# Performance work log

Measured on AMD Instinct MI355X. Metric: run time of the kernel, lower is better.

## Reference

```python
import jax, jax.numpy as jnp
import numpy as np

# Power-of-two, per-tensor, signed fake quantization (brevitas CustomQuant):
# scale = 2^ceil(log2(max|x| / int_max)), restrict POWER_OF_TWO, stats MAX,
# signed, narrow_range=False -> int range [-2^(b-1), 2^(b-1)-1].
# Weights use ROUND, activations use FLOOR (CustomSignedActQuant).

def _fake_quant(x, bits, rnd_fn):
    int_max = 2.0 ** (bits - 1) - 1.0   # 127 for 8-bit
    int_min = -(2.0 ** (bits - 1))      # -128
    max_abs = jnp.max(jnp.abs(x))
    scale = 2.0 ** jnp.ceil(jnp.log2(jnp.maximum(max_abs, 1e-10) / int_max))
    q = jnp.clip(rnd_fn(x / scale), int_min, int_max) * scale
    # straight-through estimator (quant-dequant forward, identity backward)
    return x + jax.lax.stop_gradient(q - x)


def setup_inputs() -> dict:
    key = jax.random.key(0)
    ks = jax.random.split(key, 7)
    B, C, H, W, P = 16, 728, 64, 64, 728
    x = jax.random.normal(ks[0], (B, C, H, W), jnp.float32)
    w_dw = jax.random.normal(ks[1], (C, 1, 3, 3), jnp.float32) * 0.1   # depthwise, groups=C
    w_pw = jax.random.normal(ks[2], (P, C, 1, 1), jnp.float32) * 0.05  # pointwise 1x1
    gamma = 1.0 + 0.1 * jax.random.normal(ks[3], (C,), jnp.float32)
    beta = 0.1 * jax.random.normal(ks[4], (C,), jnp.float32)
    run_mean = 0.1 * jax.random.normal(ks[5], (C,), jnp.float32)
    run_var = 0.5 + jax.random.uniform(ks[6], (C,), jnp.float32)
    return {"x": x, "w_dw": w_dw, "w_pw": w_pw, "gamma": gamma,
            "beta": beta, "run_mean": run_mean, "run_var": run_var}


def reference(x, w_dw, w_pw, gamma, beta, run_mean, run_var):
    C = x.shape[1]
    eps = 1e-5
    # fixed_padding: kernel=3, dilation=1 -> pad_total=2 -> (1,1) each side
    xp = jnp.pad(x, ((0, 0), (0, 0), (1, 1), (1, 1)))
    # quantized depthwise conv (groups = inplanes)
    wq = _fake_quant(w_dw, 8, jnp.round)
    y = jax.lax.conv_general_dilated(
        xp, wq, window_strides=(1, 1), padding='VALID',
        dimension_numbers=('NCHW', 'OIHW', 'NCHW'),
        feature_group_count=C)
    # BatchNorm2d (eval mode, running stats)
    inv = gamma / jnp.sqrt(run_var + eps)                # [C]
    y = y * inv[:, None, None] + (beta - run_mean * inv)[:, None, None]
    # quantized identity on activations (FLOOR)
    y = _fake_quant(y, 8, jnp.floor)
    # quantized pointwise 1x1 conv
    wpq = _fake_quant(w_pw, 8, jnp.round)
    out = jnp.einsum('bchw,oc->bohw', y, wpq[:, :, 0, 0])
    return out
```

## Files before the change

kernel.cpp:

```cpp
#include <hip/hip_runtime.h>

#define C_IN 728
#define NB   16
#define HH   64
#define WW   64
#define HW   4096
#define KPAD 736
#define MPAD 768

typedef __bf16 bf16x8 __attribute__((ext_vector_type(8)));
typedef float  f32x4  __attribute__((ext_vector_type(4)));

__device__ __forceinline__ float p2scale(unsigned bits, float int_max) {
    float ma = __uint_as_float(bits);
    float v = fmaxf(ma, 1e-10f) / int_max;
    int e; float m = frexpf(v, &e);
    if (m == 0.5f) e -= 1;
    return ldexpf(1.0f, e);
}

__global__ void init_slots(unsigned* slots) {
    if (threadIdx.x < 3) slots[threadIdx.x] = 0u;
}

__device__ __forceinline__ float block_max(float v) {
    #pragma unroll
    for (int off = 32; off; off >>= 1) v = fmaxf(v, __shfl_down(v, off));
    __shared__ float red[4];
    int lane = threadIdx.x & 63, wv = threadIdx.x >> 6;
    if (lane == 0) red[wv] = v;
    __syncthreads();
    return fmaxf(fmaxf(red[0], red[1]), fmaxf(red[2], red[3]));
}

__global__ __launch_bounds__(256) void maxabs_kernel(const float* __restrict__ p, int n,
                                                     unsigned* slot) {
    float v = 0.f;
    for (int i = blockIdx.x * 256 + threadIdx.x; i < n; i += gridDim.x * 256)
        v = fmaxf(v, fabsf(p[i]));
    float m = block_max(v);
    if (threadIdx.x == 0)
        atomicMax(slot, __float_as_uint(m));
}

__global__ __launch_bounds__(256) void quant_dw(const float* __restrict__ w,
                                                float* __restrict__ wq,
                                                const unsigned* __restrict__ slots) {
    int i = blockIdx.x * 256 + threadIdx.x;
    if (i >= C_IN * 9) return;
    float s = p2scale(slots[0], 127.f);
    float k = fminf(fmaxf(rintf(w[i] / s), -128.f), 127.f);
    wq[i] = k * s;
}

__global__ __launch_bounds__(256) void dwconv_bn(const float* __restrict__ x,
                                                 const float* __restrict__ wq,
                                                 const float* __restrict__ gamma,
                                                 const float* __restrict__ beta,
                                                 const float* __restrict__ rmean,
                                                 const float* __restrict__ rvar,
                                                 float* __restrict__ y,
                                                 float* __restrict__ partial) {
    __shared__ __align__(16) float tile[HW];
    const int c = blockIdx.x, b = blockIdx.y, t = threadIdx.x;
    const float* xp = x + ((size_t)b * C_IN + c) * HW;

    const float4* xv = (const float4*)xp;
    float4* tv = (float4*)tile;
    #pragma unroll
    for (int i = 0; i < 4; ++i) tv[t + i * 256] = xv[t + i * 256];

    float wk[9];
    #pragma unroll
    for (int j = 0; j < 9; ++j) wk[j] = wq[c * 9 + j];
    const float inv  = gamma[c] / sqrtf(rvar[c] + 1e-5f);
    const float bias = beta[c] - rmean[c] * inv;
    __syncthreads();

    float* yp = y + ((size_t)b * C_IN + c) * HW;
    float vmax = 0.f;
    #pragma unroll
    for (int i = 0; i < 16; ++i) {
        const int p = t + i * 256;
        const int h = p >> 6, wc = p & 63;
        float acc = 0.f;
        #pragma unroll
        for (int dh = -1; dh <= 1; ++dh) {
            const int hh = h + dh;
            if ((unsigned)hh < (unsigned)HH) {
                const int base = hh << 6;
                if (wc > 0)  acc += tile[base + wc - 1] * wk[(dh + 1) * 3 + 0];
                acc += tile[base + wc] * wk[(dh + 1) * 3 + 1];
                if (wc < 63) acc += tile[base + wc + 1] * wk[(dh + 1) * 3 + 2];
            }
        }
        const float val = acc * inv + bias;
        yp[p] = val;
        vmax = fmaxf(vmax, fabsf(val));
    }
    const float m = block_max(vmax);
    if (t == 0) partial[b * C_IN + c] = m;
}

__global__ __launch_bounds__(256) void reduce_partial(const float* __restrict__ p, int n,
                                                      unsigned* __restrict__ slot) {
    float v = 0.f;
    for (int i = threadIdx.x; i < n; i += 256) v = fmaxf(v, p[i]);
    float m = block_max(v);
    if (threadIdx.x == 0) *slot = __float_as_uint(m);
}

__global__ __launch_bounds__(256) void quant_wpw(const float* __restrict__ w,
                                                 unsigned short* __restrict__ wq,
                                                 const unsigned* __restrict__ slots) {
    int i = blockIdx.x * 256 + threadIdx.x;
    if (i >= MPAD * KPAD) return;
    int o = i / KPAD, c = i % KPAD;
    float k = 0.f;
    if (o < C_IN && c < C_IN) {
        float s = p2scale(slots[1], 127.f);
        k = fminf(fmaxf(rintf(w[o * C_IN + c] / s), -128.f), 127.f);
    }
    wq[i] = (unsigned short)(__float_as_uint(k) >> 16);
}

__global__ __launch_bounds__(256) void transpose_quant_y(const float* __restrict__ y,
                                                         unsigned short* __restrict__ yq,
                                                         const unsigned* __restrict__ slots) {
    __shared__ float tile[32][33];
    int tx = threadIdx.x & 31, ty = threadIdx.x >> 5;
    int hw0 = blockIdx.x * 32, c0 = blockIdx.y * 32, b = blockIdx.z;
    float inv_s = 1.0f / p2scale(slots[2], 127.f);

    #pragma unroll
    for (int i = 0; i < 32; i += 8) {
        int c = c0 + ty + i;
        float v = (c < C_IN) ? y[((size_t)(b * C_IN + c)) * HW + hw0 + tx] : 0.f;
        tile[ty + i][tx] = v;
    }
    __syncthreads();
    #pragma unroll
    for (int i = 0; i < 32; i += 8) {
        int hw = hw0 + ty + i;
        int c  = c0 + tx;
        float k = 0.f;
        if (c < C_IN)
            k = fminf(fmaxf(floorf(tile[tx][ty + i] * inv_s), -128.f), 127.f);
        yq[((size_t)b * HW + hw) * KPAD + c] = (unsigned short)(__float_as_uint(k) >> 16);
    }
}

__global__ __launch_bounds__(256) void gemm_kernel(const unsigned short* __restrict__ Wq,
                                                   const unsigned short* __restrict__ Yq,
                                                   float* __restrict__ out,
                                                   const unsigned* __restrict__ slots) {
    __shared__ __align__(16) unsigned short As[128 * 32];
    __shared__ __align__(16) unsigned short Bs[128 * 32];
    const int t = threadIdx.x;
    const int w = t >> 6, l = t & 63;
    const int r = l & 15, q = l >> 4;
    const int wr = w >> 1, wc = w & 1;
    const int m0 = blockIdx.y * 128;
    const int n0 = blockIdx.x * 128;
    const int b  = blockIdx.z;

    const unsigned short* Ag = Wq + (size_t)m0 * KPAD;
    const unsigned short* Bg = Yq + ((size_t)b * HW + n0) * KPAD;

    const int sm0 = t >> 2;
    const int sm1 = 64 + sm0;
    const int sko = (t & 3) * 8;

    f32x4 acc[4][4];
    #pragma unroll
    for (int i = 0; i < 4; ++i)
        #pragma unroll
        for (int j = 0; j < 4; ++j) acc[i][j] = (f32x4){0.f, 0.f, 0.f, 0.f};

    for (int k0 = 0; k0 < KPAD; k0 += 32) {
        __builtin_amdgcn_global_load_lds(
            (const __attribute__((address_space(1))) void*)(Ag + (size_t)sm0 * KPAD + k0 + sko),
            (__attribute__((address_space(3))) void*)(As + w * 512), 16, 0, 0);
        __builtin_amdgcn_global_load_lds(
            (const __attribute__((address_space(1))) void*)(Ag + (size_t)sm1 * KPAD + k0 + sko),
            (__attribute__((address_space(3))) void*)(As + 2048 + w * 512), 16, 0, 0);
        __builtin_amdgcn_global_load_lds(
            (const __attribute__((address_space(1))) void*)(Bg + (size_t)sm0 * KPAD + k0 + sko),
            (__attribute__((address_space(3))) void*)(Bs + w * 512), 16, 0, 0);
        __builtin_amdgcn_global_load_lds(
            (const __attribute__((address_space(1))) void*)(Bg + (size_t)sm1 * KPAD + k0 + sko),
            (__attribute__((address_space(3))) void*)(Bs + 2048 + w * 512), 16, 0, 0);
        __syncthreads();

        bf16x8 af[4], bfr[4];
        #pragma unroll
        for (int fm = 0; fm < 4; ++fm)
            af[fm] = *(const bf16x8*)(As + (wr * 64 + fm * 16 + r) * 32 + q * 8);
        #pragma unroll
        for (int fn = 0; fn < 4; ++fn)
            bfr[fn] = *(const bf16x8*)(Bs + (wc * 64 + fn * 16 + r) * 32 + q * 8);
        #pragma unroll
        for (int fm = 0; fm < 4; ++fm)
            #pragma unroll
            for (int fn = 0; fn < 4; ++fn)
                acc[fm][fn] = __builtin_amdgcn_mfma_f32_16x16x32_bf16(
                    af[fm], bfr[fn], acc[fm][fn], 0, 0, 0);
        __syncthreads();
    }

    const float stot = p2scale(slots[1], 127.f) * p2scale(slots[2], 127.f);
    #pragma unroll
    for (int fm = 0; fm < 4; ++fm) {
        int o = m0 + wr * 64 + fm * 16 + q * 4;
        #pragma unroll
        for (int fn = 0; fn < 4; ++fn) {
            int hw = n0 + wc * 64 + fn * 16 + r;
            float* op = out + ((size_t)b * C_IN + o) * HW + hw;
            #pragma unroll
            for (int reg = 0; reg < 4; ++reg) {
                if (o + reg < C_IN) op[(size_t)reg * HW] = acc[fm][fn][reg] * stot;
            }
        }
    }
}

extern "C" void kernel_launch(void* const* d_in, const int* in_sizes, int n_in,
                              void* d_out, int out_size, void* d_ws, size_t ws_size,
                              hipStream_t stream) {
    const float* x     = (const float*)d_in[0];
    const float* w_dw  = (const float*)d_in[1];
    const float* w_pw  = (const float*)d_in[2];
    const float* gamma = (const float*)d_in[3];
    const float* beta  = (const float*)d_in[4];
    const float* rmean = (const float*)d_in[5];
    const float* rvar  = (const float*)d_in[6];
    float* out = (float*)d_out;

    char* ws = (char*)d_ws;
    unsigned*       slots = (unsigned*)ws;
    float*          wq_dw = (float*)(ws + 256);
    unsigned short* Wq    = (unsigned short*)(ws + 26624);
    float*          y     = (float*)(ws + 1157120);
    unsigned short* Yq    = (unsigned short*)(ws + 191997952);
    float*          partial = (float*)(ws + 191997952);

    init_slots<<<dim3(1), dim3(64), 0, stream>>>(slots);
    maxabs_kernel<<<dim3(4), dim3(256), 0, stream>>>(w_dw, C_IN * 9, slots + 0);
    maxabs_kernel<<<dim3(64), dim3(256), 0, stream>>>(w_pw, C_IN * C_IN, slots + 1);
    quant_dw<<<dim3((C_IN * 9 + 255) / 256), dim3(256), 0, stream>>>(w_dw, wq_dw, slots);
    dwconv_bn<<<dim3(C_IN, NB), dim3(256), 0, stream>>>(
        x, wq_dw, gamma, beta, rmean, rvar, y, partial);
    reduce_partial<<<dim3(1), dim3(256), 0, stream>>>(partial, NB * C_IN, slots + 2);
    quant_wpw<<<dim3((MPAD * KPAD + 255) / 256), dim3(256), 0, stream>>>(w_pw, Wq, slots);
    transpose_quant_y<<<dim3(HW / 32, KPAD / 32, NB), dim3(256), 0, stream>>>(y, Yq, slots);
    gemm_kernel<<<dim3(HW / 128, MPAD / 128, NB), dim3(256), 0, stream>>>(Wq, Yq, out, slots);
}
```

Before: 606.9 us.

## Vectorize transpose-quant with swizzled LDS tile and swizzle GEMM LDS reads

The transpose_quant_y kernel now loads float4 per thread over 128-channel tiles into an XOR-swizzled shared tile and writes eight packed bf16 values per 16-byte store, in place of scalar 2-byte stores. The GEMM applies an XOR swizzle on the k-chunk offset for global-to-LDS loads and the matching fragment reads, to reduce LDS bank conflicts. Both aim to cut memory-transaction and bank-conflict overhead. The swizzle has to match exactly between writer and reader, and the grid for the transpose changes to cover KPAD with 128-wide tiles.

Measured after the change: 581.6 us. 4.2% less time.

```diff
diff --git a/kernel.cpp b/kernel.cpp
--- a/kernel.cpp
+++ b/kernel.cpp
@@ -10,6 +10,7 @@
 
 typedef __bf16 bf16x8 __attribute__((ext_vector_type(8)));
 typedef float  f32x4  __attribute__((ext_vector_type(4)));
+typedef unsigned short us8 __attribute__((ext_vector_type(8)));
 
 __device__ __forceinline__ float p2scale(unsigned bits, float int_max) {
     float ma = __uint_as_float(bits);
@@ -127,26 +128,43 @@
 __global__ __launch_bounds__(256) void transpose_quant_y(const float* __restrict__ y,
                                                          unsigned short* __restrict__ yq,
                                                          const unsigned* __restrict__ slots) {
-    __shared__ float tile[32][33];
-    int tx = threadIdx.x & 31, ty = threadIdx.x >> 5;
-    int hw0 = blockIdx.x * 32, c0 = blockIdx.y * 32, b = blockIdx.z;
-    float inv_s = 1.0f / p2scale(slots[2], 127.f);
-
-    #pragma unroll
-    for (int i = 0; i < 32; i += 8) {
-        int c = c0 + ty + i;
-        float v = (c < C_IN) ? y[((size_t)(b * C_IN + c)) * HW + hw0 + tx] : 0.f;
-        tile[ty + i][tx] = v;
+    __shared__ __align__(16) float tile[128 * 36];
+    const int t   = threadIdx.x;
+    const int hw0 = blockIdx.x * 32;
+    const int c0  = blockIdx.y * 128;
+    const int b   = blockIdx.z;
+    const float inv_s = 1.0f / p2scale(slots[2], 127.f);
+
+    #pragma unroll
+    for (int i = 0; i < 4; ++i) {
+        const int gi = i * 256 + t;
+        const int cl = gi >> 3, g = gi & 7;
+        const int c  = c0 + cl;
+        float4 v = make_float4(0.f, 0.f, 0.f, 0.f);
+        if (c < C_IN)
+            v = *(const float4*)(y + ((size_t)(b * C_IN + c)) * HW + hw0 + g * 4);
+        const int gp = g ^ ((cl >> 3) & 7);
+        *(float4*)(tile + cl * 36 + gp * 4) = v;
     }
     __syncthreads();
-    #pragma unroll
-    for (int i = 0; i < 32; i += 8) {
-        int hw = hw0 + ty + i;
-        int c  = c0 + tx;
-        float k = 0.f;
-        if (c < C_IN)
-            k = fminf(fmaxf(floorf(tile[tx][ty + i] * inv_s), -128.f), 127.f);
-        yq[((size_t)b * HW + hw) * KPAD + c] = (unsigned short)(__float_as_uint(k) >> 16);
+
+    #pragma unroll
+    for (int it = 0; it < 2; ++it) {
+        const int hw_r = (t >> 4) + it * 16;
+        const int c8   = t & 15;
+        const int c_out = c0 + c8 * 8;
+        if (c_out < KPAD) {
+            us8 pack;
+            #pragma unroll
+            for (int j = 0; j < 8; ++j) {
+                const int cl = c8 * 8 + j;
+                const int gp = (hw_r >> 2) ^ (c8 & 7);
+                const float v = tile[cl * 36 + gp * 4 + (hw_r & 3)];
+                const float k = fminf(fmaxf(floorf(v * inv_s), -128.f), 127.f);
+                pack[j] = (unsigned short)(__float_as_uint(k) >> 16);
+            }
+            *(us8*)(yq + ((size_t)b * HW + hw0 + hw_r) * KPAD + c_out) = pack;
+        }
     }
 }
 
@@ -167,9 +185,9 @@
     const unsigned short* Ag = Wq + (size_t)m0 * KPAD;
     const unsigned short* Bg = Yq + ((size_t)b * HW + n0) * KPAD;
 
-    const int sm0 = t >> 2;
-    const int sm1 = 64 + sm0;
-    const int sko = (t & 3) * 8;
+    const int srow = t >> 2;
+    const int sko  = ((t & 3) ^ ((t >> 3) & 3)) * 8;
+    const int swr  = (r >> 1) & 3;
 
     f32x4 acc[4][4];
     #pragma unroll
@@ -179,26 +197,26 @@
 
     for (int k0 = 0; k0 < KPAD; k0 += 32) {
         __builtin_amdgcn_global_load_lds(
-            (const __attribute__((address_space(1))) void*)(Ag + (size_t)sm0 * KPAD + k0 + sko),
+            (const __attribute__((address_space(1))) void*)(Ag + (size_t)srow * KPAD + k0 + sko),
             (__attribute__((address_space(3))) void*)(As + w * 512), 16, 0, 0);
         __builtin_amdgcn_global_load_lds(
-            (const __attribute__((address_space(1))) void*)(Ag + (size_t)sm1 * KPAD + k0 + sko),
+            (const __attribute__((address_space(1))) void*)(Ag + (size_t)(64 + srow) * KPAD + k0 + sko),
             (__attribute__((address_space(3))) void*)(As + 2048 + w * 512), 16, 0, 0);
         __builtin_amdgcn_global_load_lds(
-            (const __attribute__((address_space(1))) void*)(Bg + (size_t)sm0 * KPAD + k0 + sko),
+            (const __attribute__((address_space(1))) void*)(Bg + (size_t)srow * KPAD + k0 + sko),
             (__attribute__((address_space(3))) void*)(Bs + w * 512), 16, 0, 0);
         __builtin_amdgcn_global_load_lds(
-            (const __attribute__((address_space(1))) void*)(Bg + (size_t)sm1 * KPAD + k0 + sko),
+            (const __attribute__((address_space(1))) void*)(Bg + (size_t)(64 + srow) * KPAD + k0 + sko),
             (__attribute__((address_space(3))) void*)(Bs + 2048 + w * 512), 16, 0, 0);
         __syncthreads();
 
         bf16x8 af[4], bfr[4];
         #pragma unroll
         for (int fm = 0; fm < 4; ++fm)
-            af[fm] = *(const bf16x8*)(As + (wr * 64 + fm * 16 + r) * 32 + q * 8);
+            af[fm] = *(const bf16x8*)(As + (wr * 64 + fm * 16 + r) * 32 + ((q ^ swr)) * 8);
         #pragma unroll
         for (int fn = 0; fn < 4; ++fn)
-            bfr[fn] = *(const bf16x8*)(Bs + (wc * 64 + fn * 16 + r) * 32 + q * 8);
+            bfr[fn] = *(const bf16x8*)(Bs + (wc * 64 + fn * 16 + r) * 32 + ((q ^ swr)) * 8);
         #pragma unroll
         for (int fm = 0; fm < 4; ++fm)
             #pragma unroll
@@ -252,6 +270,6 @@
         x, wq_dw, gamma, beta, rmean, rvar, y, partial);
     reduce_partial<<<dim3(1), dim3(256), 0, stream>>>(partial, NB * C_IN, slots + 2);
     quant_wpw<<<dim3((MPAD * KPAD + 255) / 256), dim3(256), 0, stream>>>(w_pw, Wq, slots);
-    transpose_quant_y<<<dim3(HW / 32, KPAD / 32, NB), dim3(256), 0, stream>>>(y, Yq, slots);
+    transpose_quant_y<<<dim3(HW / 32, KPAD / 128 + 1, NB), dim3(256), 0, stream>>>(y, Yq, slots);
     gemm_kernel<<<dim3(HW / 128, MPAD / 128, NB), dim3(256), 0, stream>>>(Wq, Yq, out, slots);
 }
```
